# Kernel optimization log

Hardware: AMD Instinct MI355X
Metric: run time of the kernel (lower is better)

## Reference

```python
import jax, jax.numpy as jnp
import numpy as np

N = 100000   # nodes
E = 1600000  # edges
NF = 128     # nfeat
NH = 64      # nhid
NC = 16      # nclass
C = 1.0      # curvature
EPS = 1e-15
PROJ_EPS = 4e-3  # float32 boundary eps used by HGCN PoincareBall
SQC = C ** 0.5


def _norm(v):
    return jnp.maximum(jnp.linalg.norm(v, axis=-1, keepdims=True), EPS)


def _artanh(v):
    return jnp.arctanh(jnp.clip(v, -1.0 + 1e-7, 1.0 - 1e-7))


def proj(p):
    # clip to the open ball of radius (1-eps)/sqrt(c)
    n = _norm(p)
    maxnorm = (1.0 - PROJ_EPS) / SQC
    return jnp.where(n > maxnorm, p / n * maxnorm, p)


def expmap0(u):
    n = _norm(u)
    return jnp.tanh(SQC * n) * u / (SQC * n)


def logmap0(p):
    n = _norm(p)
    return _artanh(SQC * n) * p / (SQC * n)


def mobius_add(x, y):
    x2 = jnp.sum(x * x, axis=-1, keepdims=True)
    y2 = jnp.sum(y * y, axis=-1, keepdims=True)
    xy = jnp.sum(x * y, axis=-1, keepdims=True)
    num = (1.0 + 2.0 * C * xy + C * y2) * x + (1.0 - C * x2) * y
    den = 1.0 + 2.0 * C * xy + (C ** 2) * x2 * y2
    return num / jnp.maximum(den, EPS)


def mobius_matvec(W, p):
    # W: [out, in], p: [N, in] on the ball
    pn = _norm(p)
    mp = p @ W.T  # [N, out]
    mpn = jnp.linalg.norm(mp, axis=-1, keepdims=True)
    res = jnp.tanh(mpn / pn * _artanh(SQC * pn)) * mp / (SQC * jnp.maximum(mpn, EPS))
    return jnp.where(mpn <= EPS, jnp.zeros_like(res), res)


def setup_inputs() -> dict:
    key = jax.random.key(0)
    ks = jax.random.split(key, 16)
    inp = {
        "x": jax.random.normal(ks[0], (N, NF), dtype=jnp.float32),
        "src": jax.random.randint(ks[1], (E,), 0, N, dtype=jnp.int32),
        "dst": jax.random.randint(ks[2], (E,), 0, N, dtype=jnp.int32),
        "adj_val": jax.random.uniform(ks[3], (E,), dtype=jnp.float32) * 0.0625,
        "W1": jax.random.normal(ks[4], (NH, NF), dtype=jnp.float32) / np.sqrt(NF),
        "b1": jnp.zeros((NH,), dtype=jnp.float32),
        "W2": jax.random.normal(ks[5], (NH, NH), dtype=jnp.float32) / np.sqrt(NH),
        "b2": jnp.zeros((NH,), dtype=jnp.float32),
        "W3": jax.random.normal(ks[6], (NH, NH), dtype=jnp.float32) / np.sqrt(NH),
        "b3": jnp.zeros((NH,), dtype=jnp.float32),
        "W4": jax.random.normal(ks[7], (NH // 2, NH), dtype=jnp.float32) / np.sqrt(NH),
        "b4": jnp.zeros((NH // 2,), dtype=jnp.float32),
        "W5": jax.random.normal(ks[8], (NC, NH // 2), dtype=jnp.float32) / np.sqrt(NH // 2),
        "b5": jnp.zeros((NC,), dtype=jnp.float32),
    }
    return inp


def _hgc_layer(h, W, b, src, dst, adj_val):
    # HypLinear: mobius matvec + hyperbolic bias
    res = proj(mobius_matvec(W, h))
    hyp_b = proj(expmap0(b[None, :]))
    res = proj(mobius_add(res, hyp_b))
    # HypAgg: aggregate in tangent space at origin via sparse adj
    ht = logmap0(res)                                   # [N, d]
    msg = adj_val[:, None] * ht[src]                    # [E, d]
    agg = jax.ops.segment_sum(msg, dst, num_segments=N)  # [N, d]
    res = proj(expmap0(agg))
    # HypAct: relu in tangent space, re-map to ball
    res = proj(expmap0(jax.nn.relu(logmap0(res))))
    return res


def reference(x, src, dst, adj_val, W1, b1, W2, b2, W3, b3, W4, b4, W5, b5):
    h = proj(expmap0(x))  # map Euclidean features to the ball (proj_tan0 = identity)
    h = _hgc_layer(h, W1, b1, src, dst, adj_val)
    h = _hgc_layer(h, W2, b2, src, dst, adj_val)
    h = _hgc_layer(h, W3, b3, src, dst, adj_val)
    t = logmap0(h)  # back to tangent space for the Euclidean head
    z = jax.nn.relu(t @ W4.T + b4)
    return jax.nn.log_softmax(z @ W5.T + b5, axis=-1)  # [N, nclass]
```

## Files before the change

kernel.cpp:

```cpp
#include <hip/hip_runtime.h>
#include <hip/hip_bf16.h>
#include <hip/hip_fp16.h>
#include <math.h>

#define NFEAT 128
#define NHID  64
#define ATH996 3.106303f
#define CHUNK 4096

typedef __attribute__((ext_vector_type(8))) short short8;
typedef __attribute__((ext_vector_type(4))) float floatx4;
typedef unsigned short ushort_t;
typedef unsigned long long u64;

__device__ __forceinline__ float wave_sum(float v) {
#pragma unroll
    for (int m = 1; m < 64; m <<= 1) v += __shfl_xor(v, m, 64);
    return v;
}

__device__ __forceinline__ float fast_tanh(float x) {
    float e = __expf(2.f * x);
    return 1.f - 2.f / (e + 1.f);
}

__device__ __forceinline__ float artanh_clip(float v) {
    const float lim = 0.99999988f;
    v = fminf(fmaxf(v, -lim), lim);
    return 0.5f * __logf((1.f + v) / (1.f - v));
}

__device__ __forceinline__ unsigned pack2(float a, float b) {
    __hip_bfloat16 x = __float2bfloat16(a), y = __float2bfloat16(b);
    ushort_t ux = *(ushort_t*)&x, uy = *(ushort_t*)&y;
    return (unsigned)ux | ((unsigned)uy << 16);
}

__device__ __forceinline__ ushort_t f2bf(float f) {
    __hip_bfloat16 h = __float2bfloat16(f);
    return *(ushort_t*)&h;
}

__device__ __forceinline__ float pe_adj(unsigned p) {
    return __half2float(__ushort_as_half((ushort_t)(p & 0x7fffu)));
}


__global__ __launch_bounds__(256) void k_bscan(const int* __restrict__ gBktCnt,
        int* __restrict__ gBktBase, int* __restrict__ gCur,
        int* __restrict__ off, int nb, int n, int e) {
    __shared__ int s[256];
    int tid = threadIdx.x;
    int base = tid * 4;
    int c0 = (base + 0 < nb) ? gBktCnt[base + 0] : 0;
    int c1 = (base + 1 < nb) ? gBktCnt[base + 1] : 0;
    int c2 = (base + 2 < nb) ? gBktCnt[base + 2] : 0;
    int c3 = (base + 3 < nb) ? gBktCnt[base + 3] : 0;
    int tsum = c0 + c1 + c2 + c3;
    s[tid] = tsum; __syncthreads();
    for (int o = 1; o < 256; o <<= 1) {
        int v = (tid >= o) ? s[tid - o] : 0;
        __syncthreads();
        s[tid] += v;
        __syncthreads();
    }
    int ex = s[tid] - tsum;
    int e0 = ex, e1 = ex + c0, e2 = ex + c0 + c1, e3 = ex + c0 + c1 + c2;
    if (base + 0 < nb) { gBktBase[base + 0] = e0; gCur[base + 0] = e0; }
    if (base + 1 < nb) { gBktBase[base + 1] = e1; gCur[base + 1] = e1; }
    if (base + 2 < nb) { gBktBase[base + 2] = e2; gCur[base + 2] = e2; }
    if (base + 3 < nb) { gBktBase[base + 3] = e3; gCur[base + 3] = e3; }
    if (tid == 255) gBktBase[nb] = s[255];
    if (tid == 0) off[n] = e;
}

__global__ __launch_bounds__(256) void k_bscatter(const int* __restrict__ dst,
        const int* __restrict__ src, const float* __restrict__ adj,
        int* __restrict__ gCur, u64* __restrict__ gStage, int e, int nb) {
    __shared__ u64 stage[CHUNK];
    __shared__ int cnt[512], excl[512], rcnt[512], myBase[512], s[256];
    int tid = threadIdx.x;
    int start = blockIdx.x * CHUNK, end = min(e, start + CHUNK);
    for (int t = tid; t < nb; t += 256) { cnt[t] = 0; rcnt[t] = 0; }
    __syncthreads();
    for (int i = start + tid; i < end; i += 256)
        atomicAdd(&cnt[dst[i] >> 8], 1);
    __syncthreads();
    int v0 = (2 * tid < nb) ? cnt[2 * tid] : 0;
    int v1 = (2 * tid + 1 < nb) ? cnt[2 * tid + 1] : 0;
    int tsum = v0 + v1;
    s[tid] = tsum; __syncthreads();
    for (int o = 1; o < 256; o <<= 1) {
        int v = (tid >= o) ? s[tid - o] : 0;
        __syncthreads();
        s[tid] += v;
        __syncthreads();
    }
    int ex = s[tid] - tsum;
    if (2 * tid < nb) excl[2 * tid] = ex;
    if (2 * tid + 1 < nb) excl[2 * tid + 1] = ex + v0;
    __syncthreads();
    for (int t = tid; t < nb; t += 256)
        if (cnt[t]) myBase[t] = atomicAdd(&gCur[t], cnt[t]);
    for (int i = start + tid; i < end; i += 256) {
        int d = dst[i];
        int b = d >> 8;
        unsigned ab = (unsigned)__half_as_ushort(__float2half(adj[i])) & 0x7fffu;
        u64 u = ((u64)(unsigned)d << 32) |
                (u64)(((unsigned)src[i] << 15) | ab);
        int r = atomicAdd(&rcnt[b], 1);
        stage[excl[b] + r] = u;
    }
    __syncthreads();
    int sz = end - start;
    for (int j = tid; j < sz; j += 256) {
        u64 u = stage[j];
        int b = (int)(u >> 40) & 0x1ff;
        gStage[myBase[b] + (j - excl[b])] = u;
    }
}

__global__ __launch_bounds__(256) void k_bfinal(const u64* __restrict__ gStage,
        const int* __restrict__ gBktBase, int* __restrict__ off,
        unsigned* __restrict__ pe, int n) {
    __shared__ int ncnt[256], nexcl[256], rcnt[256], s[256];
    int tid = threadIdx.x, b = blockIdx.x;
    int ebeg = gBktBase[b], eend = gBktBase[b + 1];
    int nbeg = b << 8;
    ncnt[tid] = 0; rcnt[tid] = 0;
    __syncthreads();
    for (int j = ebeg + tid; j < eend; j += 256) {
        int dl = ((int)(gStage[j] >> 32) & 0x1ffff) - nbeg;
        atomicAdd(&ncnt[dl], 1);
    }
    __syncthreads();
    int v = ncnt[tid];
    s[tid] = v; __syncthreads();
    for (int o = 1; o < 256; o <<= 1) {
        int t2 = (tid >= o) ? s[tid - o] : 0;
        __syncthreads();
        s[tid] += t2;
        __syncthreads();
    }
    nexcl[tid] = s[tid] - v;
    if (nbeg + tid < n) off[nbeg + tid] = ebeg + nexcl[tid];
    __syncthreads();
    for (int j = ebeg + tid; j < eend; j += 256) {
        u64 u = gStage[j];
        int dl = ((int)(u >> 32) & 0x1ffff) - nbeg;
        int r = atomicAdd(&rcnt[dl], 1);
        pe[ebeg + nexcl[dl] + r] = (unsigned)u;
    }
}

__global__ __launch_bounds__(256) void k_prep(
        const float* __restrict__ W1, const float* __restrict__ W2,
        const float* __restrict__ W3, const float* __restrict__ W4,
        const float* __restrict__ W5, const float* __restrict__ b1,
        const float* __restrict__ b2, const float* __restrict__ b3,
        ushort_t* __restrict__ Bpk1, ushort_t* __restrict__ Bpk2,
        ushort_t* __restrict__ Bpk3, ushort_t* __restrict__ Bpk4,
        ushort_t* __restrict__ Bpk5, float* __restrict__ hbs,
        float* __restrict__ hbns, int* __restrict__ gBktCnt, int nb) {
    int bid = blockIdx.x, tid = threadIdx.x;
    if (bid >= 75) {
        for (int t = tid; t < nb; t += 256) gBktCnt[t] = 0;
        return;
    }
    if (bid < 64) {
        const float* W; ushort_t* Bpk; int K, o;
        if (bid < 32)      { W = W1; Bpk = Bpk1; K = 128; o = bid * 256 + tid; }
        else if (bid < 48) { W = W2; Bpk = Bpk2; K = 64;  o = (bid - 32) * 256 + tid; }
        else               { W = W3; Bpk = Bpk3; K = 64;  o = (bid - 48) * 256 + tid; }
        int j = o & 7, c = (o >> 3) & 15, nf = (o >> 7) & 3, hi = (o >> 9) & 3,
            ks = o >> 11;
        Bpk[o] = f2bf(W[(nf * 16 + c) * K + ks * 32 + hi * 8 + j]);
    } else if (bid < 72) {
        int o = (bid - 64) * 256 + tid;
        int j = o & 7, c = (o >> 3) & 15, nf = (o >> 7) & 1, hi = (o >> 8) & 3,
            ks = o >> 10;
        Bpk4[o] = f2bf(W4[(nf * 16 + c) * 64 + ks * 32 + hi * 8 + j]);
    } else if (bid < 74) {
        int o = (bid - 72) * 256 + tid;
        if (o < 512) {
            int j = o & 7, c = (o >> 3) & 15, hi = o >> 7;
            Bpk5[o] = f2bf(W5[c * 32 + hi * 8 + j]);
        }
    } else {
        if (tid < 192) {
            int wv = tid >> 6, lane = tid & 63;
            const float* b = (wv == 0) ? b1 : (wv == 1) ? b2 : b3;
            float bv = b[lane];
            float bn = fmaxf(sqrtf(wave_sum(bv * bv)), 1e-15f);
            float th = fast_tanh(bn);
            float f = th / bn;
            float hn = th;
            if (th > 0.996f) { f = 0.996f / bn; hn = 0.996f; }
            hbs[wv * 64 + lane] = bv * f;
            if (lane == 0) hbns[wv] = hn;
        }
    }
}

__device__ __forceinline__ void epi_vals(const float vin[4], float pn,
        float hbn, const float* __restrict__ hb, int c, float outv[4]) {
    float pp = 0.f;
#pragma unroll
    for (int nf = 0; nf < 4; ++nf) pp += vin[nf] * vin[nf];
#pragma unroll
    for (int m = 1; m < 16; m <<= 1) pp += __shfl_xor(pp, m, 64);
    float mpn = sqrtf(pp);
    float an = artanh_clip(pn);
    if (hbn <= 1e-15f) {
        float targ = (mpn / pn) * an;
        float scale = (targ > ATH996) ? (ATH996 / mpn) : (an / pn);
        if (mpn <= 1e-15f) scale = 0.f;
#pragma unroll
        for (int nf = 0; nf < 4; ++nf) outv[nf] = vin[nf] * scale;
    } else {
        float targ = (mpn / pn) * an;
        float th = fast_tanh(targ);
        float rn = fminf(th, 0.996f);
        float rs = (mpn <= 1e-15f) ? 0.f : (rn / mpn);
        float res[4], xyp = 0.f;
#pragma unroll
        for (int nf = 0; nf < 4; ++nf) {
            res[nf] = vin[nf] * rs;
            xyp += res[nf] * hb[nf * 16 + c];
        }
#pragma unroll
        for (int m = 1; m < 16; m <<= 1) xyp += __shfl_xor(xyp, m, 64);
        float x2 = rn * rn, y2 = hbn * hbn;
        float den = fmaxf(1.f + 2.f * xyp + x2 * y2, 1e-15f);
        float ca = (1.f + 2.f * xyp + y2) / den, cb = (1.f - x2) / den;
        float mv[4], mm = 0.f;
#pragma unroll
        for (int nf = 0; nf < 4; ++nf) {
            mv[nf] = ca * res[nf] + cb * hb[nf * 16 + c];
            mm += mv[nf] * mv[nf];
        }
#pragma unroll
        for (int m = 1; m < 16; m <<= 1) mm += __shfl_xor(mm, m, 64);
        float mn = sqrtf(mm);
        float mc = fminf(fmaxf(mn, 1e-15f), 0.996f);
        float msc = ((mn > 0.996f) ? (0.996f / mn) : 1.f) * artanh_clip(mc) / mc;
#pragma unroll
        for (int nf = 0; nf < 4; ++nf) outv[nf] = mv[nf] * msc;
    }
}

__global__ __launch_bounds__(256) void k_gemm1_hist(
        const float* __restrict__ x, const ushort_t* __restrict__ Bpk,
        const float* __restrict__ hb, const float* __restrict__ hbn_p,
        ushort_t* __restrict__ htout, int n, int gBlocks,
        const int* __restrict__ dst, int* __restrict__ gBktCnt, int e, int nb) {
    constexpr int RB = 256;
    __shared__ __align__(16) unsigned char As[64 * RB];
    __shared__ float pns[64], fs[64];
    __shared__ int cnt[512];
    int tid = threadIdx.x;
    if ((int)blockIdx.x >= gBlocks) {
        for (int t = tid; t < nb; t += 256) cnt[t] = 0;
        __syncthreads();
        int start = ((int)blockIdx.x - gBlocks) * CHUNK, end = min(e, start + CHUNK);
        for (int i = start + tid; i < end; i += 256)
            atomicAdd(&cnt[dst[i] >> 8], 1);
        __syncthreads();
        for (int t = tid; t < nb; t += 256)
            if (cnt[t]) atomicAdd(&gBktCnt[t], cnt[t]);
        return;
    }
    int wv = tid >> 6, lane = tid & 63;
    int grp = lane >> 4, l = lane & 15;
    int rowBase = blockIdx.x * 64;
#pragma unroll
    for (int it = 0; it < 4; ++it) {
        int row = wv * 16 + it * 4 + grp, rg = rowBase + row;
        float4 va = make_float4(0.f, 0.f, 0.f, 0.f), vb = va;
        if (rg < n) {
            const float4* xr = (const float4*)(x + (size_t)rg * NFEAT + l * 8);
            va = xr[0]; vb = xr[1];
        }
        uint4 pk;
        pk.x = pack2(va.x, va.y); pk.y = pack2(va.z, va.w);
        pk.z = pack2(vb.x, vb.y); pk.w = pack2(vb.z, vb.w);
        unsigned byte = (unsigned)(row * RB + l * 16) ^ ((row & 7) << 4);
        *(uint4*)(As + byte) = pk;
        float ss = va.x * va.x + va.y * va.y + va.z * va.z + va.w * va.w +
                   vb.x * vb.x + vb.y * vb.y + vb.z * vb.z + vb.w * vb.w;
#pragma unroll
        for (int m = 1; m < 16; m <<= 1) ss += __shfl_xor(ss, m, 64);
        if (l == 0) {
            float nr = fmaxf(sqrtf(ss), 1e-15f);
            float th = fast_tanh(nr);
            float f = th / nr;
            float pn = fmaxf(th, 1e-15f);
            if (th > 0.996f) { f = 0.996f / nr; pn = 0.996f; }
            pns[row] = pn; fs[row] = f;
        }
    }
    int hi = lane >> 4, c = lane & 15;
    short8 bf[4][4];
#pragma unroll
    for (int ks = 0; ks < 4; ++ks)
#pragma unroll
        for (int nf = 0; nf < 4; ++nf)
            bf[ks][nf] = *(const short8*)(Bpk + (((size_t)(ks * 4 + hi) * 4 + nf) * 16 + c) * 8);
    floatx4 acc[4];
#pragma unroll
    for (int nf = 0; nf < 4; ++nf)
#pragma unroll
        for (int r = 0; r < 4; ++r) acc[nf][r] = 0.f;
    int arow = wv * 16 + c;
#pragma unroll
    for (int ks = 0; ks < 4; ++ks) {
        unsigned byte = (unsigned)(arow * RB + ks * 64 + hi * 16) ^ ((arow & 7) << 4);
        short8 af = *(const short8*)(As + byte);
#pragma unroll
        for (int nf = 0; nf < 4; ++nf)
            acc[nf] = __builtin_amdgcn_mfma_f32_16x16x32_bf16(af, bf[ks][nf], acc[nf], 0, 0, 0);
    }
    float hbn = hbn_p[0];
#pragma unroll
    for (int r = 0; r < 4; ++r) {
        int row = wv * 16 + hi * 4 + r, rg = rowBase + row;
        float f = fs[row];
        float vin[4], outv[4];
#pragma unroll
        for (int nf = 0; nf < 4; ++nf) vin[nf] = acc[nf][r] * f;
        epi_vals(vin, pns[row], hbn, hb, c, outv);
        if (rg < n) {
#pragma unroll
            for (int nf = 0; nf < 4; ++nf)
                htout[(size_t)rg * 64 + nf * 16 + c] = f2bf(outv[nf]);
        }
    }
}

__global__ __launch_bounds__(256) void k_gemm64(
        const ushort_t* __restrict__ h, const float* __restrict__ nrm_in,
        const ushort_t* __restrict__ Bpk, const float* __restrict__ hb,
        const float* __restrict__ hbn_p, ushort_t* __restrict__ htout, int n) {
    constexpr int RB = 128;
    __shared__ __align__(16) unsigned char As[64 * RB];
    int tid = threadIdx.x, wv = tid >> 6, lane = tid & 63;
    int grp = lane >> 4, l = lane & 15;
    int rowBase = blockIdx.x * 64;
#pragma unroll
    for (int it = 0; it < 4; ++it) {
        int row = wv * 16 + it * 4 + grp, rg = rowBase + row;
        uint2 pk = make_uint2(0u, 0u);
        if (rg < n) pk = *(const uint2*)(h + (size_t)rg * 64 + l * 4);
        unsigned byte = (unsigned)(row * RB + l * 8) ^ ((row & 7) << 4);
        *(uint2*)(As + byte) = pk;
    }
    int hi = lane >> 4, c = lane & 15;
    short8 bf[2][4];
#pragma unroll
    for (int ks = 0; ks < 2; ++ks)
#pragma unroll
        for (int nf = 0; nf < 4; ++nf)
            bf[ks][nf] = *(const short8*)(Bpk + (((size_t)(ks * 4 + hi) * 4 + nf) * 16 + c) * 8);
    floatx4 acc[4];
#pragma unroll
    for (int nf = 0; nf < 4; ++nf)
#pragma unroll
        for (int r = 0; r < 4; ++r) acc[nf][r] = 0.f;
    int arow = wv * 16 + c;
#pragma unroll
    for (int ks = 0; ks < 2; ++ks) {
        unsigned byte = (unsigned)(arow * RB + ks * 64 + hi * 16) ^ ((arow & 7) << 4);
        short8 af = *(const short8*)(As + byte);
#pragma unroll
        for (int nf = 0; nf < 4; ++nf)
            acc[nf] = __builtin_amdgcn_mfma_f32_16x16x32_bf16(af, bf[ks][nf], acc[nf], 0, 0, 0);
    }
    float hbn = hbn_p[0];
#pragma unroll
    for (int r = 0; r < 4; ++r) {
        int row = wv * 16 + hi * 4 + r, rg = rowBase + row;
        float pn = (rg < n) ? nrm_in[rg] : 1e-15f;
        float vin[4], outv[4];
#pragma unroll
        for (int nf = 0; nf < 4; ++nf) vin[nf] = acc[nf][r];
        epi_vals(vin, pn, hbn, hb, c, outv);
        if (rg < n) {
#pragma unroll
            for (int nf = 0; nf < 4; ++nf)
                htout[(size_t)rg * 64 + nf * 16 + c] = f2bf(outv[nf]);
        }
    }
}

template <bool TANGENT_OUT>
__global__ __launch_bounds__(256) void k_agg_act(
        const ushort_t* __restrict__ ht, const int* __restrict__ off,
        const unsigned* __restrict__ pe, ushort_t* __restrict__ hout,
        float* __restrict__ nrm_out, int n) {
    int tid = threadIdx.x;
    int grp = tid >> 4, l = tid & 15;
    int node = blockIdx.x * 16 + grp;
    if (node >= n) return;
    int beg = off[node], end = off[node + 1];
    const char* hb8 = (const char*)ht + l * 8;
    float a0[4] = {0.f, 0.f, 0.f, 0.f};
    float a1[4] = {0.f, 0.f, 0.f, 0.f};
    float a2[4] = {0.f, 0.f, 0.f, 0.f};
    float a3[4] = {0.f, 0.f, 0.f, 0.f};
    int e = beg;
    for (; e + 3 < end; e += 4) {
        unsigned p0 = pe[e], p1 = pe[e + 1], p2 = pe[e + 2], p3 = pe[e + 3];
        uint2 r0 = *(const uint2*)(hb8 + ((size_t)(p0 >> 15) << 7));
        uint2 r1 = *(const uint2*)(hb8 + ((size_t)(p1 >> 15) << 7));
        uint2 r2 = *(const uint2*)(hb8 + ((size_t)(p2 >> 15) << 7));
        uint2 r3 = *(const uint2*)(hb8 + ((size_t)(p3 >> 15) << 7));
        float w0 = pe_adj(p0), w1 = pe_adj(p1), w2 = pe_adj(p2), w3 = pe_adj(p3);
        a0[0] = fmaf(w0, __uint_as_float(r0.x << 16), a0[0]);
        a0[1] = fmaf(w0, __uint_as_float(r0.x & 0xffff0000u), a0[1]);
        a0[2] = fmaf(w0, __uint_as_float(r0.y << 16), a0[2]);
        a0[3] = fmaf(w0, __uint_as_float(r0.y & 0xffff0000u), a0[3]);
        a1[0] = fmaf(w1, __uint_as_float(r1.x << 16), a1[0]);
        a1[1] = fmaf(w1, __uint_as_float(r1.x & 0xffff0000u), a1[1]);
        a1[2] = fmaf(w1, __uint_as_float(r1.y << 16), a1[2]);
        a1[3] = fmaf(w1, __uint_as_float(r1.y & 0xffff0000u), a1[3]);
        a2[0] = fmaf(w2, __uint_as_float(r2.x << 16), a2[0]);
        a2[1] = fmaf(w2, __uint_as_float(r2.x & 0xffff0000u), a2[1]);
        a2[2] = fmaf(w2, __uint_as_float(r2.y << 16), a2[2]);
        a2[3] = fmaf(w2, __uint_as_float(r2.y & 0xffff0000u), a2[3]);
        a3[0] = fmaf(w3, __uint_as_float(r3.x << 16), a3[0]);
        a3[1] = fmaf(w3, __uint_as_float(r3.x & 0xffff0000u), a3[1]);
        a3[2] = fmaf(w3, __uint_as_float(r3.y << 16), a3[2]);
        a3[3] = fmaf(w3, __uint_as_float(r3.y & 0xffff0000u), a3[3]);
    }
    for (; e < end; ++e) {
        unsigned p = pe[e];
        uint2 r = *(const uint2*)(hb8 + ((size_t)(p >> 15) << 7));
        float w = pe_adj(p);
        a0[0] = fmaf(w, __uint_as_float(r.x << 16), a0[0]);
        a0[1] = fmaf(w, __uint_as_float(r.x & 0xffff0000u), a0[1]);
        a0[2] = fmaf(w, __uint_as_float(r.y << 16), a0[2]);
        a0[3] = fmaf(w, __uint_as_float(r.y & 0xffff0000u), a0[3]);
    }
    float f0 = (a0[0] + a1[0]) + (a2[0] + a3[0]);
    float f1 = (a0[1] + a1[1]) + (a2[1] + a3[1]);
    float f2 = (a0[2] + a1[2]) + (a2[2] + a3[2]);
    float f3 = (a0[3] + a1[3]) + (a2[3] + a3[3]);
    float ss = f0 * f0 + f1 * f1 + f2 * f2 + f3 * f3;
#pragma unroll
    for (int m = 1; m < 16; m <<= 1) ss += __shfl_xor(ss, m, 64);
    float un = fmaxf(sqrtf(ss), 1e-15f);
    float thu = fast_tanh(un);
    float pf = thu / un, pn = thu;
    if (thu > 0.996f) { pf = 0.996f / un; pn = 0.996f; }
    float pnc = fmaxf(pn, 1e-15f);
    float ls = artanh_clip(pnc) / pnc * pf;
    float t0 = fmaxf(ls * f0, 0.f), t1 = fmaxf(ls * f1, 0.f);
    float t2 = fmaxf(ls * f2, 0.f), t3 = fmaxf(ls * f3, 0.f);
    float ss2 = t0 * t0 + t1 * t1 + t2 * t2 + t3 * t3;
#pragma unroll
    for (int m = 1; m < 16; m <<= 1) ss2 += __shfl_xor(ss2, m, 64);
    float tn = fmaxf(sqrtf(ss2), 1e-15f);
    uint2 ov;
    if (TANGENT_OUT) {
        float sc = (tn > ATH996) ? (ATH996 / tn) : 1.f;
        ov = make_uint2(pack2(t0 * sc, t1 * sc), pack2(t2 * sc, t3 * sc));
    } else {
        float tht = fast_tanh(tn);
        float rf = tht / tn, rn = tht;
        if (tht > 0.996f) { rf = 0.996f / tn; rn = 0.996f; }
        ov = make_uint2(pack2(rf * t0, rf * t1), pack2(rf * t2, rf * t3));
        if (l == 0) nrm_out[node] = fmaxf(rn, 1e-15f);
    }
    *(uint2*)((char*)hout + (size_t)node * 128 + l * 8) = ov;
}

__global__ __launch_bounds__(256) void k_head(
        const ushort_t* __restrict__ t_in, const ushort_t* __restrict__ Bpk4,
        const float* __restrict__ b4, const ushort_t* __restrict__ Bpk5,
        const float* __restrict__ b5, float* __restrict__ out, int n) {
    constexpr int RB = 128;
    __shared__ __align__(16) unsigned char As[64 * RB];
    __shared__ __align__(16) unsigned char Zs[4][16 * 80];
    int tid = threadIdx.x, wv = tid >> 6, lane = tid & 63;
    int grp = lane >> 4, l = lane & 15;
    int rowBase = blockIdx.x * 64;
#pragma unroll
    for (int it = 0; it < 4; ++it) {
        int row = wv * 16 + it * 4 + grp, rg = rowBase + row;
        uint2 pk = make_uint2(0u, 0u);
        if (rg < n) pk = *(const uint2*)(t_in + (size_t)rg * 64 + l * 4);
        unsigned byte = (unsigned)(row * RB + l * 8) ^ ((row & 7) << 4);
        *(uint2*)(As + byte) = pk;
    }
    int hi = lane >> 4, c = lane & 15;
    short8 bf4[2][2];
#pragma unroll
    for (int ks = 0; ks < 2; ++ks)
#pragma unroll
        for (int nf = 0; nf < 2; ++nf)
            bf4[ks][nf] = *(const short8*)(Bpk4 + (((size_t)(ks * 4 + hi) * 2 + nf) * 16 + c) * 8);
    floatx4 acc[2];
#pragma unroll
    for (int nf = 0; nf < 2; ++nf)
#pragma unroll
        for (int r = 0; r < 4; ++r) acc[nf][r] = 0.f;
    int arow = wv * 16 + c;
#pragma unroll
    for (int ks = 0; ks < 2; ++ks) {
        unsigned byte = (unsigned)(arow * RB + ks * 64 + hi * 16) ^ ((arow & 7) << 4);
        short8 af = *(const short8*)(As + byte);
#pragma unroll
        for (int nf = 0; nf < 2; ++nf)
            acc[nf] = __builtin_amdgcn_mfma_f32_16x16x32_bf16(af, bf4[ks][nf], acc[nf], 0, 0, 0);
    }
    float bb0 = b4[c], bb1 = b4[16 + c];
#pragma unroll
    for (int r = 0; r < 4; ++r) {
        int zr = hi * 4 + r;
        *(ushort_t*)(Zs[wv] + zr * 80 + c * 2) = f2bf(fmaxf(acc[0][r] + bb0, 0.f));
        *(ushort_t*)(Zs[wv] + zr * 80 + (16 + c) * 2) = f2bf(fmaxf(acc[1][r] + bb1, 0.f));
    }
    short8 bf5 = *(const short8*)(Bpk5 + ((size_t)(hi * 16 + c)) * 8);
    short8 zf = *(const short8*)(Zs[wv] + c * 80 + hi * 16);
    floatx4 acc5;
#pragma unroll
    for (int r = 0; r < 4; ++r) acc5[r] = 0.f;
    acc5 = __builtin_amdgcn_mfma_f32_16x16x32_bf16(zf, bf5, acc5, 0, 0, 0);
    float b5v = b5[c];
#pragma unroll
    for (int r = 0; r < 4; ++r) {
        float y = acc5[r] + b5v;
        float mx = y;
#pragma unroll
        for (int mk = 1; mk < 16; mk <<= 1) mx = fmaxf(mx, __shfl_xor(mx, mk, 64));
        float sm = __expf(y - mx);
#pragma unroll
        for (int mk = 1; mk < 16; mk <<= 1) sm += __shfl_xor(sm, mk, 64);
        int rg = rowBase + wv * 16 + hi * 4 + r;
        if (rg < n) out[(size_t)rg * 16 + c] = y - mx - __logf(sm);
    }
}

extern "C" void kernel_launch(void* const* d_in, const int* in_sizes, int n_in,
                              void* d_out, int out_size, void* d_ws, size_t ws_size,
                              hipStream_t stream) {
    const float* x   = (const float*)d_in[0];
    const int*   src = (const int*)d_in[1];
    const int*   dst = (const int*)d_in[2];
    const float* adj = (const float*)d_in[3];
    const float* W1  = (const float*)d_in[4];  const float* b1 = (const float*)d_in[5];
    const float* W2  = (const float*)d_in[6];  const float* b2 = (const float*)d_in[7];
    const float* W3  = (const float*)d_in[8];  const float* b3 = (const float*)d_in[9];
    const float* W4  = (const float*)d_in[10]; const float* b4 = (const float*)d_in[11];
    const float* W5  = (const float*)d_in[12]; const float* b5 = (const float*)d_in[13];
    float* out = (float*)d_out;

    const int N = in_sizes[0] / NFEAT;
    const int E = in_sizes[1];
    const int NB = (N + 255) >> 8;

    char* w = (char*)d_ws;
    auto alloc = [&](size_t bytes) {
        char* p = w; w += (bytes + 255) & ~(size_t)255; return p;
    };
    int* off      = (int*)alloc((size_t)(N + 1) * 4);
    int* gBktCnt  = (int*)alloc((size_t)NB * 4);
    int* gBktBase = (int*)alloc((size_t)(NB + 1) * 4);
    int* gCur     = (int*)alloc((size_t)NB * 4);
    u64* gStage   = (u64*)alloc((size_t)E * 8);
    unsigned* pe  = (unsigned*)alloc((size_t)E * 4);
    ushort_t* B   = (ushort_t*)alloc((size_t)N * 64 * 2);
    ushort_t* D   = (ushort_t*)alloc((size_t)N * 64 * 2);
    float* nrm    = (float*)alloc((size_t)N * 4);
    float* hbs    = (float*)alloc(192 * 4);
    float* hbns   = (float*)alloc(4 * 4);
    ushort_t* Bpk1 = (ushort_t*)alloc(8192 * 2);
    ushort_t* Bpk2 = (ushort_t*)alloc(4096 * 2);
    ushort_t* Bpk3 = (ushort_t*)alloc(4096 * 2);
    ushort_t* Bpk4 = (ushort_t*)alloc(2048 * 2);
    ushort_t* Bpk5 = (ushort_t*)alloc(512 * 2);

    dim3 blk(256);
    int aggBlocks  = (N + 15) / 16;
    int gemmBlocks = (N + 63) / 64;
    int sortBlocks = (E + CHUNK - 1) / CHUNK;

    k_prep<<<76, blk, 0, stream>>>(W1, W2, W3, W4, W5, b1, b2, b3,
                                   Bpk1, Bpk2, Bpk3, Bpk4, Bpk5, hbs, hbns,
                                   gBktCnt, NB);

    k_gemm1_hist<<<gemmBlocks + sortBlocks, blk, 0, stream>>>(
        x, Bpk1, hbs, hbns, B, N, gemmBlocks, dst, gBktCnt, E, NB);

    k_bscan<<<1, blk, 0, stream>>>(gBktCnt, gBktBase, gCur, off, NB, N, E);
    k_bscatter<<<sortBlocks, blk, 0, stream>>>(dst, src, adj, gCur, gStage, E, NB);
    k_bfinal<<<NB, blk, 0, stream>>>(gStage, gBktBase, off, pe, N);

    k_agg_act<false><<<aggBlocks, blk, 0, stream>>>(B, off, pe, D, nrm, N);
    k_gemm64<<<gemmBlocks, blk, 0, stream>>>(D, nrm, Bpk2, hbs + 64, hbns + 1, B, N);
    k_agg_act<false><<<aggBlocks, blk, 0, stream>>>(B, off, pe, D, nrm, N);
    k_gemm64<<<gemmBlocks, blk, 0, stream>>>(D, nrm, Bpk3, hbs + 128, hbns + 2, B, N);
    k_agg_act<true><<<aggBlocks, blk, 0, stream>>>(B, off, pe, D, nullptr, N);

    k_head<<<gemmBlocks, blk, 0, stream>>>(D, Bpk4, b4, Bpk5, b5, out, N);
}
```

Before: 218.7 us.

## Fuse neighbor aggregation and activation into the following 64x64 GEMM kernel

Layers 2 and 3 now run in one kernel. It gathers and aggregates neighbor features, applies the hyperbolic activation, stages the 16 resulting rows in LDS and runs the MFMA matmul and epilogue in the same block. This drops the intermediate feature and norm arrays round-tripping through global memory and removes two launches. The price is that each of the four waves computes the same 16x64 MFMA tile redundantly. The gather loops are also unrolled from 4 to 8 edges to keep more loads in flight.

```diff
diff --git a/kernel.cpp b/kernel.cpp
--- a/kernel.cpp
+++ b/kernel.cpp
@@ -337,23 +337,80 @@
     }
 }
 
-__global__ __launch_bounds__(256) void k_gemm64(
-        const ushort_t* __restrict__ h, const float* __restrict__ nrm_in,
-        const ushort_t* __restrict__ Bpk, const float* __restrict__ hb,
-        const float* __restrict__ hbn_p, ushort_t* __restrict__ htout, int n) {
+__global__ __launch_bounds__(256) void k_agg_gemm(
+        const ushort_t* __restrict__ ht, const int* __restrict__ off,
+        const unsigned* __restrict__ pe, const ushort_t* __restrict__ Bpk,
+        const float* __restrict__ hb, const float* __restrict__ hbn_p,
+        ushort_t* __restrict__ htout, int n) {
     constexpr int RB = 128;
-    __shared__ __align__(16) unsigned char As[64 * RB];
-    int tid = threadIdx.x, wv = tid >> 6, lane = tid & 63;
-    int grp = lane >> 4, l = lane & 15;
-    int rowBase = blockIdx.x * 64;
-#pragma unroll
-    for (int it = 0; it < 4; ++it) {
-        int row = wv * 16 + it * 4 + grp, rg = rowBase + row;
-        uint2 pk = make_uint2(0u, 0u);
-        if (rg < n) pk = *(const uint2*)(h + (size_t)rg * 64 + l * 4);
-        unsigned byte = (unsigned)(row * RB + l * 8) ^ ((row & 7) << 4);
-        *(uint2*)(As + byte) = pk;
-    }
+    __shared__ __align__(16) unsigned char As[16 * RB];
+    __shared__ float pns[16];
+    int tid = threadIdx.x;
+    int grp = tid >> 4, l = tid & 15;
+    int node = blockIdx.x * 16 + grp;
+    float h0 = 0.f, h1 = 0.f, h2 = 0.f, h3 = 0.f, rn = 1e-15f;
+    if (node < n) {
+        int beg = off[node], end = off[node + 1];
+        const char* hb8 = (const char*)ht + l * 8;
+        float ac[4][4] = {};
+        int e = beg;
+        for (; e + 7 < end; e += 8) {
+            unsigned p[8];
+#pragma unroll
+            for (int u = 0; u < 8; ++u) p[u] = pe[e + u];
+            uint2 rr[8];
+#pragma unroll
+            for (int u = 0; u < 8; ++u)
+                rr[u] = *(const uint2*)(hb8 + ((size_t)(p[u] >> 15) << 7));
+#pragma unroll
+            for (int u = 0; u < 8; ++u) {
+                float w = pe_adj(p[u]);
+                ac[u & 3][0] = fmaf(w, __uint_as_float(rr[u].x << 16), ac[u & 3][0]);
+                ac[u & 3][1] = fmaf(w, __uint_as_float(rr[u].x & 0xffff0000u), ac[u & 3][1]);
+                ac[u & 3][2] = fmaf(w, __uint_as_float(rr[u].y << 16), ac[u & 3][2]);
+                ac[u & 3][3] = fmaf(w, __uint_as_float(rr[u].y & 0xffff0000u), ac[u & 3][3]);
+            }
+        }
+        for (; e < end; ++e) {
+            unsigned p = pe[e];
+            uint2 r = *(const uint2*)(hb8 + ((size_t)(p >> 15) << 7));
+            float w = pe_adj(p);
+            ac[0][0] = fmaf(w, __uint_as_float(r.x << 16), ac[0][0]);
+            ac[0][1] = fmaf(w, __uint_as_float(r.x & 0xffff0000u), ac[0][1]);
+            ac[0][2] = fmaf(w, __uint_as_float(r.y << 16), ac[0][2]);
+            ac[0][3] = fmaf(w, __uint_as_float(r.y & 0xffff0000u), ac[0][3]);
+        }
+        float f0 = (ac[0][0] + ac[1][0]) + (ac[2][0] + ac[3][0]);
+        float f1 = (ac[0][1] + ac[1][1]) + (ac[2][1] + ac[3][1]);
+        float f2 = (ac[0][2] + ac[1][2]) + (ac[2][2] + ac[3][2]);
+        float f3 = (ac[0][3] + ac[1][3]) + (ac[2][3] + ac[3][3]);
+        float ss = f0 * f0 + f1 * f1 + f2 * f2 + f3 * f3;
+#pragma unroll
+        for (int m = 1; m < 16; m <<= 1) ss += __shfl_xor(ss, m, 64);
+        float un = fmaxf(sqrtf(ss), 1e-15f);
+        float thu = fast_tanh(un);
+        float pf = thu / un, pn = thu;
+        if (thu > 0.996f) { pf = 0.996f / un; pn = 0.996f; }
+        float pnc = fmaxf(pn, 1e-15f);
+        float ls = artanh_clip(pnc) / pnc * pf;
+        float t0 = fmaxf(ls * f0, 0.f), t1 = fmaxf(ls * f1, 0.f);
+        float t2 = fmaxf(ls * f2, 0.f), t3 = fmaxf(ls * f3, 0.f);
+        float ss2 = t0 * t0 + t1 * t1 + t2 * t2 + t3 * t3;
+#pragma unroll
+        for (int m = 1; m < 16; m <<= 1) ss2 += __shfl_xor(ss2, m, 64);
+        float tn = fmaxf(sqrtf(ss2), 1e-15f);
+        float tht = fast_tanh(tn);
+        float rf = tht / tn;
+        rn = tht;
+        if (tht > 0.996f) { rf = 0.996f / tn; rn = 0.996f; }
+        rn = fmaxf(rn, 1e-15f);
+        h0 = rf * t0; h1 = rf * t1; h2 = rf * t2; h3 = rf * t3;
+    }
+    unsigned byte = (unsigned)(grp * RB + l * 8) ^ ((grp & 7) << 4);
+    *(uint2*)(As + byte) = make_uint2(pack2(h0, h1), pack2(h2, h3));
+    if (l == 0) pns[grp] = rn;
+    __syncthreads();
+    int wv = tid >> 6, lane = tid & 63;
     int hi = lane >> 4, c = lane & 15;
     short8 bf[2][4];
 #pragma unroll
@@ -366,85 +423,71 @@
     for (int nf = 0; nf < 4; ++nf)
 #pragma unroll
         for (int r = 0; r < 4; ++r) acc[nf][r] = 0.f;
-    int arow = wv * 16 + c;
+    int arow = c;
 #pragma unroll
     for (int ks = 0; ks < 2; ++ks) {
-        unsigned byte = (unsigned)(arow * RB + ks * 64 + hi * 16) ^ ((arow & 7) << 4);
-        short8 af = *(const short8*)(As + byte);
+        unsigned ab = (unsigned)(arow * RB + ks * 64 + hi * 16) ^ ((arow & 7) << 4);
+        short8 af = *(const short8*)(As + ab);
 #pragma unroll
         for (int nf = 0; nf < 4; ++nf)
             acc[nf] = __builtin_amdgcn_mfma_f32_16x16x32_bf16(af, bf[ks][nf], acc[nf], 0, 0, 0);
     }
     float hbn = hbn_p[0];
-#pragma unroll
-    for (int r = 0; r < 4; ++r) {
-        int row = wv * 16 + hi * 4 + r, rg = rowBase + row;
-        float pn = (rg < n) ? nrm_in[rg] : 1e-15f;
-        float vin[4], outv[4];
-#pragma unroll
-        for (int nf = 0; nf < 4; ++nf) vin[nf] = acc[nf][r];
-        epi_vals(vin, pn, hbn, hb, c, outv);
-        if (rg < n) {
-#pragma unroll
-            for (int nf = 0; nf < 4; ++nf)
-                htout[(size_t)rg * 64 + nf * 16 + c] = f2bf(outv[nf]);
-        }
-    }
-}
-
-template <bool TANGENT_OUT>
-__global__ __launch_bounds__(256) void k_agg_act(
+    int r = wv;
+    int row = hi * 4 + r, rg = blockIdx.x * 16 + row;
+    float pn = pns[row];
+    float vin[4], outv[4];
+#pragma unroll
+    for (int nf = 0; nf < 4; ++nf) vin[nf] = acc[nf][r];
+    epi_vals(vin, pn, hbn, hb, c, outv);
+    if (rg < n) {
+#pragma unroll
+        for (int nf = 0; nf < 4; ++nf)
+            htout[(size_t)rg * 64 + nf * 16 + c] = f2bf(outv[nf]);
+    }
+}
+
+__global__ __launch_bounds__(256) void k_agg_tan(
         const ushort_t* __restrict__ ht, const int* __restrict__ off,
-        const unsigned* __restrict__ pe, ushort_t* __restrict__ hout,
-        float* __restrict__ nrm_out, int n) {
+        const unsigned* __restrict__ pe, ushort_t* __restrict__ hout, int n) {
     int tid = threadIdx.x;
     int grp = tid >> 4, l = tid & 15;
     int node = blockIdx.x * 16 + grp;
     if (node >= n) return;
     int beg = off[node], end = off[node + 1];
     const char* hb8 = (const char*)ht + l * 8;
-    float a0[4] = {0.f, 0.f, 0.f, 0.f};
-    float a1[4] = {0.f, 0.f, 0.f, 0.f};
-    float a2[4] = {0.f, 0.f, 0.f, 0.f};
-    float a3[4] = {0.f, 0.f, 0.f, 0.f};
+    float ac[4][4] = {};
     int e = beg;
-    for (; e + 3 < end; e += 4) {
-        unsigned p0 = pe[e], p1 = pe[e + 1], p2 = pe[e + 2], p3 = pe[e + 3];
-        uint2 r0 = *(const uint2*)(hb8 + ((size_t)(p0 >> 15) << 7));
-        uint2 r1 = *(const uint2*)(hb8 + ((size_t)(p1 >> 15) << 7));
-        uint2 r2 = *(const uint2*)(hb8 + ((size_t)(p2 >> 15) << 7));
-        uint2 r3 = *(const uint2*)(hb8 + ((size_t)(p3 >> 15) << 7));
-        float w0 = pe_adj(p0), w1 = pe_adj(p1), w2 = pe_adj(p2), w3 = pe_adj(p3);
-        a0[0] = fmaf(w0, __uint_as_float(r0.x << 16), a0[0]);
-        a0[1] = fmaf(w0, __uint_as_float(r0.x & 0xffff0000u), a0[1]);
-        a0[2] = fmaf(w0, __uint_as_float(r0.y << 16), a0[2]);
-        a0[3] = fmaf(w0, __uint_as_float(r0.y & 0xffff0000u), a0[3]);
-        a1[0] = fmaf(w1, __uint_as_float(r1.x << 16), a1[0]);
-        a1[1] = fmaf(w1, __uint_as_float(r1.x & 0xffff0000u), a1[1]);
-        a1[2] = fmaf(w1, __uint_as_float(r1.y << 16), a1[2]);
-        a1[3] = fmaf(w1, __uint_as_float(r1.y & 0xffff0000u), a1[3]);
-        a2[0] = fmaf(w2, __uint_as_float(r2.x << 16), a2[0]);
-        a2[1] = fmaf(w2, __uint_as_float(r2.x & 0xffff0000u), a2[1]);
-        a2[2] = fmaf(w2, __uint_as_float(r2.y << 16), a2[2]);
-        a2[3] = fmaf(w2, __uint_as_float(r2.y & 0xffff0000u), a2[3]);
-        a3[0] = fmaf(w3, __uint_as_float(r3.x << 16), a3[0]);
-        a3[1] = fmaf(w3, __uint_as_float(r3.x & 0xffff0000u), a3[1]);
-        a3[2] = fmaf(w3, __uint_as_float(r3.y << 16), a3[2]);
-        a3[3] = fmaf(w3, __uint_as_float(r3.y & 0xffff0000u), a3[3]);
+    for (; e + 7 < end; e += 8) {
+        unsigned p[8];
+#pragma unroll
+        for (int u = 0; u < 8; ++u) p[u] = pe[e + u];
+        uint2 rr[8];
+#pragma unroll
+        for (int u = 0; u < 8; ++u)
+            rr[u] = *(const uint2*)(hb8 + ((size_t)(p[u] >> 15) << 7));
+#pragma unroll
+        for (int u = 0; u < 8; ++u) {
+            float w = pe_adj(p[u]);
+            ac[u & 3][0] = fmaf(w, __uint_as_float(rr[u].x << 16), ac[u & 3][0]);
+            ac[u & 3][1] = fmaf(w, __uint_as_float(rr[u].x & 0xffff0000u), ac[u & 3][1]);
+            ac[u & 3][2] = fmaf(w, __uint_as_float(rr[u].y << 16), ac[u & 3][2]);
+            ac[u & 3][3] = fmaf(w, __uint_as_float(rr[u].y & 0xffff0000u), ac[u & 3][3]);
+        }
     }
     for (; e < end; ++e) {
         unsigned p = pe[e];
         uint2 r = *(const uint2*)(hb8 + ((size_t)(p >> 15) << 7));
         float w = pe_adj(p);
-        a0[0] = fmaf(w, __uint_as_float(r.x << 16), a0[0]);
-        a0[1] = fmaf(w, __uint_as_float(r.x & 0xffff0000u), a0[1]);
-        a0[2] = fmaf(w, __uint_as_float(r.y << 16), a0[2]);
-        a0[3] = fmaf(w, __uint_as_float(r.y & 0xffff0000u), a0[3]);
-    }
-    float f0 = (a0[0] + a1[0]) + (a2[0] + a3[0]);
-    float f1 = (a0[1] + a1[1]) + (a2[1] + a3[1]);
-    float f2 = (a0[2] + a1[2]) + (a2[2] + a3[2]);
-    float f3 = (a0[3] + a1[3]) + (a2[3] + a3[3]);
+        ac[0][0] = fmaf(w, __uint_as_float(r.x << 16), ac[0][0]);
+        ac[0][1] = fmaf(w, __uint_as_float(r.x & 0xffff0000u), ac[0][1]);
+        ac[0][2] = fmaf(w, __uint_as_float(r.y << 16), ac[0][2]);
+        ac[0][3] = fmaf(w, __uint_as_float(r.y & 0xffff0000u), ac[0][3]);
+    }
+    float f0 = (ac[0][0] + ac[1][0]) + (ac[2][0] + ac[3][0]);
+    float f1 = (ac[0][1] + ac[1][1]) + (ac[2][1] + ac[3][1]);
+    float f2 = (ac[0][2] + ac[1][2]) + (ac[2][2] + ac[3][2]);
+    float f3 = (ac[0][3] + ac[1][3]) + (ac[2][3] + ac[3][3]);
     float ss = f0 * f0 + f1 * f1 + f2 * f2 + f3 * f3;
 #pragma unroll
     for (int m = 1; m < 16; m <<= 1) ss += __shfl_xor(ss, m, 64);
@@ -460,17 +503,8 @@
 #pragma unroll
     for (int m = 1; m < 16; m <<= 1) ss2 += __shfl_xor(ss2, m, 64);
     float tn = fmaxf(sqrtf(ss2), 1e-15f);
-    uint2 ov;
-    if (TANGENT_OUT) {
-        float sc = (tn > ATH996) ? (ATH996 / tn) : 1.f;
-        ov = make_uint2(pack2(t0 * sc, t1 * sc), pack2(t2 * sc, t3 * sc));
-    } else {
-        float tht = fast_tanh(tn);
-        float rf = tht / tn, rn = tht;
-        if (tht > 0.996f) { rf = 0.996f / tn; rn = 0.996f; }
-        ov = make_uint2(pack2(rf * t0, rf * t1), pack2(rf * t2, rf * t3));
-        if (l == 0) nrm_out[node] = fmaxf(rn, 1e-15f);
-    }
+    float sc = (tn > ATH996) ? (ATH996 / tn) : 1.f;
+    uint2 ov = make_uint2(pack2(t0 * sc, t1 * sc), pack2(t2 * sc, t3 * sc));
     *(uint2*)((char*)hout + (size_t)node * 128 + l * 8) = ov;
 }
 
@@ -571,7 +605,6 @@
     unsigned* pe  = (unsigned*)alloc((size_t)E * 4);
     ushort_t* B   = (ushort_t*)alloc((size_t)N * 64 * 2);
     ushort_t* D   = (ushort_t*)alloc((size_t)N * 64 * 2);
-    float* nrm    = (float*)alloc((size_t)N * 4);
     float* hbs    = (float*)alloc(192 * 4);
     float* hbns   = (float*)alloc(4 * 4);
     ushort_t* Bpk1 = (ushort_t*)alloc(8192 * 2);
@@ -596,11 +629,11 @@
     k_bscatter<<<sortBlocks, blk, 0, stream>>>(dst, src, adj, gCur, gStage, E, NB);
     k_bfinal<<<NB, blk, 0, stream>>>(gStage, gBktBase, off, pe, N);
 
-    k_agg_act<false><<<aggBlocks, blk, 0, stream>>>(B, off, pe, D, nrm, N);
-    k_gemm64<<<gemmBlocks, blk, 0, stream>>>(D, nrm, Bpk2, hbs + 64, hbns + 1, B, N);
-    k_agg_act<false><<<aggBlocks, blk, 0, stream>>>(B, off, pe, D, nrm, N);
-    k_gemm64<<<gemmBlocks, blk, 0, stream>>>(D, nrm, Bpk3, hbs + 128, hbns + 2, B, N);
-    k_agg_act<true><<<aggBlocks, blk, 0, stream>>>(B, off, pe, D, nullptr, N);
+    k_agg_gemm<<<aggBlocks, blk, 0, stream>>>(B, off, pe, Bpk2,
+                                              hbs + 64, hbns + 1, D, N);
+    k_agg_gemm<<<aggBlocks, blk, 0, stream>>>(D, off, pe, Bpk3,
+                                              hbs + 128, hbns + 2, B, N);
+    k_agg_tan<<<aggBlocks, blk, 0, stream>>>(B, off, pe, D, N);
 
     k_head<<<gemmBlocks, blk, 0, stream>>>(D, Bpk4, b4, Bpk5, b5, out, N);
 }
```

Result: no change. 219.9 us (+0.6%).
